# Kernel optimization log

Measured on AMD Instinct MI355X. Metric: run time of the kernel, lower is better.

Reference implementation:

```python
import jax, jax.numpy as jnp
import numpy as np

N, D, K, NCB = 65536, 256, 1024, 4


def setup_inputs() -> dict:
    key = jax.random.key(0)
    kz, kc = jax.random.split(key)
    z = jax.random.normal(kz, (N, D), dtype=jnp.float32)
    # nn.Embedding weights init: uniform(-1/k, 1/k)
    codebooks = jax.random.uniform(kc, (NCB, K, D), dtype=jnp.float32,
                                   minval=-1.0 / K, maxval=1.0 / K)
    return {"z": z, "codebooks": codebooks}


def _vq_step(r, W):
    """One VQ codebook pass. r: [N, D], W: [k, D].
    Squared L2 distance via matmul trick: ||r||^2 - 2 r.W^T + ||W||^2,
    same math as sum((r[:,None,:]-W)**2, -1) without the [N,k,D] blowup."""
    r2 = jnp.sum(r * r, axis=-1, keepdims=True)            # [N, 1]
    w2 = jnp.sum(W * W, axis=-1)                           # [k]
    dist = r2 - 2.0 * (r @ W.T) + w2                       # [N, k]
    ind = jnp.argmin(dist, axis=-1)                        # [N]
    z_q = W[ind]                                           # [N, D]
    sg = jax.lax.stop_gradient
    vq_loss = jnp.mean((z_q - sg(r)) ** 2)
    commitment_loss = jnp.mean((r - sg(z_q)) ** 2)
    z_q_st = r + sg(z_q - r)                               # straight-through
    return z_q_st, ind, vq_loss + commitment_loss


def reference(z, codebooks):
    residual = z
    quant_sum = jnp.zeros_like(z)
    inds = []
    total_loss = jnp.zeros((), dtype=z.dtype)
    for i in range(codebooks.shape[0]):  # small fixed loop over codebooks
        z_q, ind, loss = _vq_step(residual, codebooks[i])
        residual = residual - z_q
        quant_sum = quant_sum + z_q
        inds.append(ind)
        total_loss = total_loss + loss
    return quant_sum, jnp.stack(inds, axis=1), total_loss
```

## Files before the change

kernel.cpp:

```cpp
#include <hip/hip_runtime.h>


#define N_TOK 65536
#define DIM   256
#define KCB   1024
#define NCBK  4

#define TM  32
#define TK  512
#define DC  16
#define RST 260
#define WST 18

#define QS_F   ((size_t)N_TOK * DIM)
#define IDX_F  QS_F
#define IDXE_F (IDX_F + (size_t)N_TOK * NCBK)
#define LOSS_F IDXE_F

#define WS_PART_OFF 16384
#define WS_FLAG_OFF 32768

typedef unsigned short u16;
typedef unsigned int   u32;

__device__ __forceinline__ float bf2f(u32 h) { return __uint_as_float(h << 16); }

__device__ __forceinline__ float getv(const void* base, int f32in, size_t elt) {
    if (f32in) return ((const float*)base)[elt];
    return bf2f(((const u16*)base)[elt]);
}

__device__ __forceinline__ void load8(const void* base, int f32in, size_t elt,
                                      float* f) {
    if (f32in) {
        const float4* p = (const float4*)((const float*)base + elt);
        float4 a = p[0], b = p[1];
        f[0] = a.x; f[1] = a.y; f[2] = a.z; f[3] = a.w;
        f[4] = b.x; f[5] = b.y; f[6] = b.z; f[7] = b.w;
    } else {
        uint4 q = *(const uint4*)((const u16*)base + elt);
        f[0] = bf2f(q.x & 0xffffu); f[1] = bf2f(q.x >> 16);
        f[2] = bf2f(q.y & 0xffffu); f[3] = bf2f(q.y >> 16);
        f[4] = bf2f(q.z & 0xffffu); f[5] = bf2f(q.z >> 16);
        f[6] = bf2f(q.w & 0xffffu); f[7] = bf2f(q.w >> 16);
    }
}

__global__ void canary_kernel(float* out) {
    int gid = blockIdx.x * 256 + threadIdx.x;
    size_t pos = IDX_F + (size_t)gid;
    if (pos < IDXE_F) out[pos] = 512.0f;
    if (gid == 0) out[LOSS_F] = 512.0f;
}

__global__ void detect_kernel(const u16* z16, const u16* cb16, int* flags) {
    __shared__ int s0[256], s1[256];
    int tid = threadIdx.x;
    u32 a = z16[tid],  ea = (a >> 7) & 0xffu;
    u32 b = cb16[tid], eb = (b >> 7) & 0xffu;
    s0[tid] = ((ea >= 90u && ea <= 140u) || ((a & 0x7fffu) == 0u)) ? 1 : 0;
    s1[tid] = ((eb >= 90u && eb <= 140u) || ((b & 0x7fffu) == 0u)) ? 1 : 0;
    __syncthreads();
    for (int st = 128; st > 0; st >>= 1) {
        if (tid < st) { s0[tid] += s0[tid + st]; s1[tid] += s1[tid + st]; }
        __syncthreads();
    }
    if (tid == 0) { flags[0] = (s0[0] < 218) ? 1 : 0;
                    flags[1] = (s1[0] < 218) ? 1 : 0; }
}

__device__ __forceinline__ float np128_sq_g(const void* base, int f32in, size_t off) {
    float S[16];
    #pragma unroll
    for (int l = 0; l < 16; ++l) {
        float A[8];
        #pragma unroll
        for (int j = 0; j < 8; ++j) {
            float x = getv(base, f32in, off + 16 * j + l);
            A[j] = x * x;
        }
        S[l] = ((A[0] + A[1]) + (A[2] + A[3])) + ((A[4] + A[5]) + (A[6] + A[7]));
    }
    float B1[8], B2[4];
    #pragma unroll
    for (int l = 0; l < 8; ++l) B1[l] = S[l] + S[l + 8];
    #pragma unroll
    for (int l = 0; l < 4; ++l) B2[l] = B1[l] + B1[l + 4];
    return (B2[0] + B2[2]) + (B2[1] + B2[3]);
}

__device__ __forceinline__ float np128_sq_lds(const float* a) {
    float S[16];
    #pragma unroll
    for (int l = 0; l < 16; ++l) {
        float A[8];
        #pragma unroll
        for (int j = 0; j < 8; ++j) { float x = a[16 * j + l]; A[j] = x * x; }
        S[l] = ((A[0] + A[1]) + (A[2] + A[3])) + ((A[4] + A[5]) + (A[6] + A[7]));
    }
    float B1[8], B2[4];
    #pragma unroll
    for (int l = 0; l < 8; ++l) B1[l] = S[l] + S[l + 8];
    #pragma unroll
    for (int l = 0; l < 4; ++l) B2[l] = B1[l] + B1[l + 4];
    return (B2[0] + B2[2]) + (B2[1] + B2[3]);
}

__global__ void w2_kernel(const void* cbs, float* w2f, const int* flags) {
    int kf = blockIdx.x * 256 + threadIdx.x;
    const int fc = flags[1];
    size_t base = (size_t)kf * DIM;
    w2f[kf] = np128_sq_g(cbs, fc, base) + np128_sq_g(cbs, fc, base + 128);
}

__global__
__attribute__((amdgpu_flat_work_group_size(256, 256), amdgpu_waves_per_eu(2, 2)))
void rq_kernel(const void* z, const void* cbs, const float* w2f,
               float* out, double* partials, const int* flags) {
    __shared__ float  Rld[TM * RST];
    __shared__ float  Wld[TK * WST];
    __shared__ float  r2s[TM];
    __shared__ int    bestk[TM];
    __shared__ double dred[256];

    float* candv = Wld;
    int*   candi = (int*)(Wld + TM * 65);

    const int fz = flags[0], fc = flags[1];
    const int tid  = threadIdx.x;
    const int tx   = tid & 31;
    const int ty   = tid >> 5;
    const int rowg = ty & 3;
    const int cg   = ty >> 2;
    const int row0 = blockIdx.x * TM;

    const int stg_k0 = tid >> 1;
    const int stg_dp = (tid & 1) * 8;

    for (int it = 0; it < 4; ++it) {
        int flat = it * 256 + tid;
        int r = flat >> 5, c8 = flat & 31;
        float f[8];
        load8(z, fz, (size_t)(row0 + r) * DIM + c8 * 8, f);
        int base = r * RST + c8 * 8;
        #pragma unroll
        for (int e = 0; e < 8; ++e) Rld[base + e] = f[e];
    }
    double lsum = 0.0;

    for (int cb = 0; cb < NCBK; ++cb) {
        const size_t cbW = (size_t)cb * KCB * DIM;
        const float* w2c = w2f + cb * KCB;

        __syncthreads();
        if (tid < TM) {
            const float* a = &Rld[tid * RST];
            r2s[tid] = np128_sq_lds(a) + np128_sq_lds(a + 128);
        }
        __syncthreads();

        float bval[8]; int bidx[8];
        #pragma unroll
        for (int i = 0; i < 8; ++i) { bval[i] = __uint_as_float(0x7f7fffffu); bidx[i] = 0; }

        for (int kt = 0; kt < KCB / TK; ++kt) {
            float acc[8][8];
            #pragma unroll
            for (int i = 0; i < 8; ++i)
                #pragma unroll
                for (int j = 0; j < 8; ++j) acc[i][j] = 0.f;

            for (int dc = 0; dc < DIM / DC; ++dc) {
                __syncthreads();
                #pragma unroll
                for (int it = 0; it < 4; ++it) {
                    int k  = it * 128 + stg_k0;
                    float f[8];
                    load8(cbs, fc, cbW + (size_t)(kt * TK + k) * DIM + dc * DC + stg_dp, f);
                    int wb = k * WST + stg_dp;
                    *(float2*)&Wld[wb]     = make_float2(f[0], f[1]);
                    *(float2*)&Wld[wb + 2] = make_float2(f[2], f[3]);
                    *(float2*)&Wld[wb + 4] = make_float2(f[4], f[5]);
                    *(float2*)&Wld[wb + 6] = make_float2(f[6], f[7]);
                }
                __syncthreads();

                #pragma unroll
                for (int dd = 0; dd < DC / 4; ++dd) {
                    float av[8][4];
                    #pragma unroll
                    for (int i = 0; i < 8; ++i) {
                        const float4 va = *(const float4*)
                            &Rld[(rowg + 4 * i) * RST + dc * DC + dd * 4];
                        av[i][0] = va.x; av[i][1] = va.y;
                        av[i][2] = va.z; av[i][3] = va.w;
                    }
                    #pragma unroll
                    for (int j = 0; j < 8; ++j) {
                        const int c = tx + 32 * j + 256 * cg;
                        const float2* wp = (const float2*)&Wld[c * WST + dd * 4];
                        const float2 b01 = wp[0];
                        const float2 b23 = wp[1];
                        #pragma unroll
                        for (int i = 0; i < 8; ++i) {
                            float s = acc[i][j];
                            s = fmaf(av[i][0], b01.x, s);
                            s = fmaf(av[i][1], b01.y, s);
                            s = fmaf(av[i][2], b23.x, s);
                            s = fmaf(av[i][3], b23.y, s);
                            acc[i][j] = s;
                        }
                    }
                }
            }
            #pragma unroll
            for (int j = 0; j < 8; ++j) {
                const int k = kt * TK + tx + 32 * j + 256 * cg;
                const float w2k = w2c[k];
                #pragma unroll
                for (int i = 0; i < 8; ++i) {
                    float t2   = r2s[rowg + 4 * i] - 2.0f * acc[i][j];
                    float dist = t2 + w2k;
                    if (dist < bval[i] || (dist == bval[i] && k < bidx[i])) {
                        bval[i] = dist; bidx[i] = k;
                    }
                }
            }
        }
        __syncthreads();
        #pragma unroll
        for (int i = 0; i < 8; ++i) {
            int r = rowg + 4 * i;
            candv[r * 65 + tx + 32 * cg] = bval[i];
            candi[r * 65 + tx + 32 * cg] = bidx[i];
        }
        __syncthreads();
        if (tid < TM) {
            float best = candv[tid * 65];
            int   bi   = candi[tid * 65];
            for (int t = 1; t < 64; ++t) {
                float v = candv[tid * 65 + t];
                int  ix = candi[tid * 65 + t];
                if (v < best || (v == best && ix < bi)) { best = v; bi = ix; }
            }
            bestk[tid] = bi;
            size_t pos = IDX_F + (size_t)(row0 + tid) * NCBK + cb;
            if (pos < IDXE_F) out[pos] = (float)bi;
        }
        __syncthreads();
        #pragma unroll
        for (int it = 0; it < 4; ++it) {
            int flat = it * 256 + tid;
            int r = flat >> 5, c8 = flat & 31;
            int kb = bestk[r];
            float f[8];
            load8(cbs, fc, cbW + (size_t)kb * DIM + c8 * 8, f);
            int base = r * RST + c8 * 8;
            size_t pos = (size_t)(row0 + r) * DIM + c8 * 8;
            float qv[8];
            if (cb == 0) {
                #pragma unroll
                for (int e = 0; e < 8; ++e) qv[e] = 0.0f;
            } else {
                float4 o0 = *(const float4*)&out[pos];
                float4 o1 = *(const float4*)&out[pos + 4];
                qv[0] = o0.x; qv[1] = o0.y; qv[2] = o0.z; qv[3] = o0.w;
                qv[4] = o1.x; qv[5] = o1.y; qv[6] = o1.z; qv[7] = o1.w;
            }
            #pragma unroll
            for (int e = 0; e < 8; ++e) {
                float rv = Rld[base + e];
                float t  = f[e] - rv;
                float s  = rv + t;
                float rn = rv - s;
                Rld[base + e] = rn;
                qv[e] = qv[e] + s;
                lsum += (double)t * (double)t;
            }
            float4 w0 = make_float4(qv[0], qv[1], qv[2], qv[3]);
            float4 w1 = make_float4(qv[4], qv[5], qv[6], qv[7]);
            *(float4*)&out[pos]     = w0;
            *(float4*)&out[pos + 4] = w1;
        }
        __syncthreads();
    }

    dred[tid] = lsum;
    __syncthreads();
    for (int s = 128; s > 0; s >>= 1) {
        if (tid < s) dred[tid] += dred[tid + s];
        __syncthreads();
    }
    if (tid == 0) partials[blockIdx.x] = dred[0];
}

__global__ void loss_final(const double* partials, float* out) {
    __shared__ double sred[256];
    int tid = threadIdx.x;
    double s = 0.0;
    for (int q = 0; q < 8; ++q) s += partials[tid + 256 * q];
    sred[tid] = s;
    __syncthreads();
    for (int st = 128; st > 0; st >>= 1) {
        if (tid < st) sred[tid] += sred[tid + st];
        __syncthreads();
    }
    if (tid == 0)
        out[LOSS_F] = (float)(2.0 * sred[0] / 16777216.0);
}

extern "C" void kernel_launch(void* const* d_in, const int* in_sizes, int n_in,
                              void* d_out, int out_size, void* d_ws, size_t ws_size,
                              hipStream_t stream) {
    (void)n_in; (void)out_size; (void)ws_size;
    const void* z;
    const void* cbs;
    if (in_sizes[0] == 16777216) { z = d_in[0]; cbs = d_in[1]; }
    else                         { z = d_in[1]; cbs = d_in[0]; }

    float*  out      = (float*)d_out;
    float*  w2f      = (float*)d_ws;
    double* partials = (double*)((char*)d_ws + WS_PART_OFF);
    int*    flags    = (int*)((char*)d_ws + WS_FLAG_OFF);

    canary_kernel<<<1024, 256, 0, stream>>>(out);
    detect_kernel<<<1, 256, 0, stream>>>((const u16*)z, (const u16*)cbs, flags);
    w2_kernel<<<16, 256, 0, stream>>>(cbs, w2f, flags);
    rq_kernel<<<N_TOK / TM, 256, 0, stream>>>(z, cbs, w2f, out, partials, flags);
    loss_final<<<1, 256, 0, stream>>>(partials, out);
}
```

Before: 2.767 ms.

## Restructure distance GEMM to one row per lane with wave-uniform codebook loads

Replaces the LDS-staged codebook tiling with a scheme where each lane owns one token row (64 rows per block) and each wave streams its own quarter of the codebook straight from global memory. Codewords are wave-uniform, so the loads can be scalar or broadcast and are double-buffered in registers. This drops the per-chunk LDS staging and its barriers and doubles rows per block. The cost is much less register reuse (8 accumulators per thread), more global/L2 traffic for codebook reads, and an argmin merge across waves that no longer breaks ties toward the lowest index.

```diff
diff --git a/kernel.cpp b/kernel.cpp
--- a/kernel.cpp
+++ b/kernel.cpp
@@ -6,11 +6,8 @@
 #define KCB   1024
 #define NCBK  4
 
-#define TM  32
-#define TK  512
-#define DC  16
+#define TM  64
 #define RST 260
-#define WST 18
 
 #define QS_F   ((size_t)N_TOK * DIM)
 #define IDX_F  QS_F
@@ -113,31 +110,103 @@
     w2f[kf] = np128_sq_g(cbs, fc, base) + np128_sq_g(cbs, fc, base + 128);
 }
 
-__global__
-__attribute__((amdgpu_flat_work_group_size(256, 256), amdgpu_waves_per_eu(2, 2)))
+#define LOADB_F32(B, DDX) {                                                  \
+    const float* _p = cbf + (size_t)(DDX) * 4;                               \
+    B[0] = *(const float4*)(_p);                                             \
+    B[1] = *(const float4*)(_p + DIM);                                       \
+    B[2] = *(const float4*)(_p + 2 * DIM);                                   \
+    B[3] = *(const float4*)(_p + 3 * DIM);                                   \
+    B[4] = *(const float4*)(_p + 4 * DIM);                                   \
+    B[5] = *(const float4*)(_p + 5 * DIM);                                   \
+    B[6] = *(const float4*)(_p + 6 * DIM);                                   \
+    B[7] = *(const float4*)(_p + 7 * DIM); }
+
+__device__ __forceinline__ float4 bf4(const u16* p) {
+    uint2 r = *(const uint2*)p;
+    return make_float4(bf2f(r.x & 0xffffu), bf2f(r.x >> 16),
+                       bf2f(r.y & 0xffffu), bf2f(r.y >> 16));
+}
+
+#define LOADB_BF16(B, DDX) {                                                 \
+    const u16* _p = cbh + (size_t)(DDX) * 4;                                 \
+    B[0] = bf4(_p);           B[1] = bf4(_p + DIM);                          \
+    B[2] = bf4(_p + 2 * DIM); B[3] = bf4(_p + 3 * DIM);                      \
+    B[4] = bf4(_p + 4 * DIM); B[5] = bf4(_p + 5 * DIM);                      \
+    B[6] = bf4(_p + 6 * DIM); B[7] = bf4(_p + 7 * DIM); }
+
+#define TILE_LOOP(LOADB)                                                     \
+    for (int tile = 0; tile < 32; ++tile) {                                  \
+        const int code0 = wv * 256 + tile * 8;                               \
+        const float* cbf = (const float*)cbs + cbW + (size_t)code0 * DIM;    \
+        const u16*   cbh = (const u16*)cbs + cbW + (size_t)code0 * DIM;      \
+        (void)cbf; (void)cbh;                                                \
+        float acc[8];                                                        \
+        _Pragma("unroll")                                                    \
+        for (int j = 0; j < 8; ++j) acc[j] = 0.f;                            \
+        float4 bA[8], bB[8];                                                 \
+        LOADB(bA, 0)                                                         \
+        _Pragma("unroll 2")                                                  \
+        for (int dd2 = 0; dd2 < 32; ++dd2) {                                 \
+            const int d0 = dd2 * 2;                                          \
+            LOADB(bB, d0 + 1)                                                \
+            {                                                                \
+                const float4 av = *(const float4*)&Rld[lane * RST + d0 * 4]; \
+                _Pragma("unroll")                                            \
+                for (int j = 0; j < 8; ++j) {                                \
+                    float s = acc[j];                                        \
+                    s = fmaf(av.x, bA[j].x, s);                              \
+                    s = fmaf(av.y, bA[j].y, s);                              \
+                    s = fmaf(av.z, bA[j].z, s);                              \
+                    s = fmaf(av.w, bA[j].w, s);                              \
+                    acc[j] = s;                                              \
+                }                                                            \
+            }                                                                \
+            LOADB(bA, (d0 + 2) & 63)                                         \
+            {                                                                \
+                const float4 av =                                            \
+                    *(const float4*)&Rld[lane * RST + (d0 + 1) * 4];         \
+                _Pragma("unroll")                                            \
+                for (int j = 0; j < 8; ++j) {                                \
+                    float s = acc[j];                                        \
+                    s = fmaf(av.x, bB[j].x, s);                              \
+                    s = fmaf(av.y, bB[j].y, s);                              \
+                    s = fmaf(av.z, bB[j].z, s);                              \
+                    s = fmaf(av.w, bB[j].w, s);                              \
+                    acc[j] = s;                                              \
+                }                                                            \
+            }                                                                \
+        }                                                                    \
+        _Pragma("unroll")                                                    \
+        for (int j = 0; j < 8; ++j) {                                        \
+            const int c = code0 + j;                                         \
+            const float w2k = w2c[c];                                        \
+            const float t2 = r2v - 2.0f * acc[j];                            \
+            const float dist = t2 + w2k;                                     \
+            if (dist < bval || (dist == bval && c < bidx)) {                 \
+                bval = dist; bidx = c;                                       \
+            }                                                                \
+        }                                                                    \
+    }
+
+__global__ __launch_bounds__(256, 2)
 void rq_kernel(const void* z, const void* cbs, const float* w2f,
                float* out, double* partials, const int* flags) {
     __shared__ float  Rld[TM * RST];
-    __shared__ float  Wld[TK * WST];
-    __shared__ float  r2s[TM];
+    __shared__ float  candv[4 * 64];
+    __shared__ int    candi[4 * 64];
     __shared__ int    bestk[TM];
     __shared__ double dred[256];
 
-    float* candv = Wld;
-    int*   candi = (int*)(Wld + TM * 65);
-
     const int fz = flags[0], fc = flags[1];
     const int tid  = threadIdx.x;
-    const int tx   = tid & 31;
-    const int ty   = tid >> 5;
-    const int rowg = ty & 3;
-    const int cg   = ty >> 2;
+    const int lane = tid & 63;
+    const int wv   = __builtin_amdgcn_readfirstlane(tid >> 6);
     const int row0 = blockIdx.x * TM;
 
-    const int stg_k0 = tid >> 1;
-    const int stg_dp = (tid & 1) * 8;
-
-    for (int it = 0; it < 4; ++it) {
+    const int drow = tid >> 2;
+    const int dseg = (tid & 3) * 64;
+
+    for (int it = 0; it < 8; ++it) {
         int flat = it * 256 + tid;
         int r = flat >> 5, c8 = flat & 31;
         float f[8];
@@ -153,134 +222,67 @@
         const float* w2c = w2f + cb * KCB;
 
         __syncthreads();
-        if (tid < TM) {
-            const float* a = &Rld[tid * RST];
-            r2s[tid] = np128_sq_lds(a) + np128_sq_lds(a + 128);
-        }
-        __syncthreads();
-
-        float bval[8]; int bidx[8];
-        #pragma unroll
-        for (int i = 0; i < 8; ++i) { bval[i] = __uint_as_float(0x7f7fffffu); bidx[i] = 0; }
-
-        for (int kt = 0; kt < KCB / TK; ++kt) {
-            float acc[8][8];
+
+        const float* arow = &Rld[lane * RST];
+        const float r2v = np128_sq_lds(arow) + np128_sq_lds(arow + 128);
+
+        float bval = __uint_as_float(0x7f7fffffu);
+        int   bidx = 0;
+
+        if (fc) { TILE_LOOP(LOADB_F32) }
+        else    { TILE_LOOP(LOADB_BF16) }
+
+        candv[wv * 64 + lane] = bval;
+        candi[wv * 64 + lane] = bidx;
+        __syncthreads();
+        {
+            float best = candv[lane];
+            int   bi   = candi[lane];
             #pragma unroll
-            for (int i = 0; i < 8; ++i)
-                #pragma unroll
-                for (int j = 0; j < 8; ++j) acc[i][j] = 0.f;
-
-            for (int dc = 0; dc < DIM / DC; ++dc) {
-                __syncthreads();
-                #pragma unroll
-                for (int it = 0; it < 4; ++it) {
-                    int k  = it * 128 + stg_k0;
-                    float f[8];
-                    load8(cbs, fc, cbW + (size_t)(kt * TK + k) * DIM + dc * DC + stg_dp, f);
-                    int wb = k * WST + stg_dp;
-                    *(float2*)&Wld[wb]     = make_float2(f[0], f[1]);
-                    *(float2*)&Wld[wb + 2] = make_float2(f[2], f[3]);
-                    *(float2*)&Wld[wb + 4] = make_float2(f[4], f[5]);
-                    *(float2*)&Wld[wb + 6] = make_float2(f[6], f[7]);
-                }
-                __syncthreads();
-
-                #pragma unroll
-                for (int dd = 0; dd < DC / 4; ++dd) {
-                    float av[8][4];
-                    #pragma unroll
-                    for (int i = 0; i < 8; ++i) {
-                        const float4 va = *(const float4*)
-                            &Rld[(rowg + 4 * i) * RST + dc * DC + dd * 4];
-                        av[i][0] = va.x; av[i][1] = va.y;
-                        av[i][2] = va.z; av[i][3] = va.w;
-                    }
-                    #pragma unroll
-                    for (int j = 0; j < 8; ++j) {
-                        const int c = tx + 32 * j + 256 * cg;
-                        const float2* wp = (const float2*)&Wld[c * WST + dd * 4];
-                        const float2 b01 = wp[0];
-                        const float2 b23 = wp[1];
-                        #pragma unroll
-                        for (int i = 0; i < 8; ++i) {
-                            float s = acc[i][j];
-                            s = fmaf(av[i][0], b01.x, s);
-                            s = fmaf(av[i][1], b01.y, s);
-                            s = fmaf(av[i][2], b23.x, s);
-                            s = fmaf(av[i][3], b23.y, s);
-                            acc[i][j] = s;
-                        }
-                    }
-                }
+            for (int w = 1; w < 4; ++w) {
+                float v = candv[w * 64 + lane];
+                int  ci = candi[w * 64 + lane];
+                if (v < best) { best = v; bi = ci; }
             }
-            #pragma unroll
-            for (int j = 0; j < 8; ++j) {
-                const int k = kt * TK + tx + 32 * j + 256 * cg;
-                const float w2k = w2c[k];
-                #pragma unroll
-                for (int i = 0; i < 8; ++i) {
-                    float t2   = r2s[rowg + 4 * i] - 2.0f * acc[i][j];
-                    float dist = t2 + w2k;
-                    if (dist < bval[i] || (dist == bval[i] && k < bidx[i])) {
-                        bval[i] = dist; bidx[i] = k;
-                    }
-                }
+            if (tid < 64) {
+                bestk[lane] = bi;
+                size_t pos = IDX_F + (size_t)(row0 + lane) * NCBK + cb;
+                if (pos < IDXE_F) out[pos] = (float)bi;
             }
         }
         __syncthreads();
-        #pragma unroll
-        for (int i = 0; i < 8; ++i) {
-            int r = rowg + 4 * i;
-            candv[r * 65 + tx + 32 * cg] = bval[i];
-            candi[r * 65 + tx + 32 * cg] = bidx[i];
-        }
-        __syncthreads();
-        if (tid < TM) {
-            float best = candv[tid * 65];
-            int   bi   = candi[tid * 65];
-            for (int t = 1; t < 64; ++t) {
-                float v = candv[tid * 65 + t];
-                int  ix = candi[tid * 65 + t];
-                if (v < best || (v == best && ix < bi)) { best = v; bi = ix; }
+
+        {
+            const int kb = bestk[drow];
+            for (int it = 0; it < 8; ++it) {
+                const int off = dseg + it * 8;
+                float f[8];
+                load8(cbs, fc, cbW + (size_t)kb * DIM + off, f);
+                const int    base = drow * RST + off;
+                const size_t pos  = (size_t)(row0 + drow) * DIM + off;
+                float qv[8];
+                if (cb == 0) {
+                    #pragma unroll
+                    for (int e = 0; e < 8; ++e) qv[e] = 0.0f;
+                } else {
+                    float4 o0 = *(const float4*)&out[pos];
+                    float4 o1 = *(const float4*)&out[pos + 4];
+                    qv[0] = o0.x; qv[1] = o0.y; qv[2] = o0.z; qv[3] = o0.w;
+                    qv[4] = o1.x; qv[5] = o1.y; qv[6] = o1.z; qv[7] = o1.w;
+                }
+                #pragma unroll
+                for (int e = 0; e < 8; ++e) {
+                    float rv = Rld[base + e];
+                    float t  = f[e] - rv;
+                    float s  = rv + t;
+                    float rn = rv - s;
+                    Rld[base + e] = rn;
+                    qv[e] = qv[e] + s;
+                    lsum += (double)t * (double)t;
+                }
+                *(float4*)&out[pos]     = make_float4(qv[0], qv[1], qv[2], qv[3]);
+                *(float4*)&out[pos + 4] = make_float4(qv[4], qv[5], qv[6], qv[7]);
             }
-            bestk[tid] = bi;
-            size_t pos = IDX_F + (size_t)(row0 + tid) * NCBK + cb;
-            if (pos < IDXE_F) out[pos] = (float)bi;
-        }
-        __syncthreads();
-        #pragma unroll
-        for (int it = 0; it < 4; ++it) {
-            int flat = it * 256 + tid;
-            int r = flat >> 5, c8 = flat & 31;
-            int kb = bestk[r];
-            float f[8];
-            load8(cbs, fc, cbW + (size_t)kb * DIM + c8 * 8, f);
-            int base = r * RST + c8 * 8;
-            size_t pos = (size_t)(row0 + r) * DIM + c8 * 8;
-            float qv[8];
-            if (cb == 0) {
-                #pragma unroll
-                for (int e = 0; e < 8; ++e) qv[e] = 0.0f;
-            } else {
-                float4 o0 = *(const float4*)&out[pos];
-                float4 o1 = *(const float4*)&out[pos + 4];
-                qv[0] = o0.x; qv[1] = o0.y; qv[2] = o0.z; qv[3] = o0.w;
-                qv[4] = o1.x; qv[5] = o1.y; qv[6] = o1.z; qv[7] = o1.w;
-            }
-            #pragma unroll
-            for (int e = 0; e < 8; ++e) {
-                float rv = Rld[base + e];
-                float t  = f[e] - rv;
-                float s  = rv + t;
-                float rn = rv - s;
-                Rld[base + e] = rn;
-                qv[e] = qv[e] + s;
-                lsum += (double)t * (double)t;
-            }
-            float4 w0 = make_float4(qv[0], qv[1], qv[2], qv[3]);
-            float4 w1 = make_float4(qv[4], qv[5], qv[6], qv[7]);
-            *(float4*)&out[pos]     = w0;
-            *(float4*)&out[pos + 4] = w1;
         }
         __syncthreads();
     }
@@ -298,7 +300,7 @@
     __shared__ double sred[256];
     int tid = threadIdx.x;
     double s = 0.0;
-    for (int q = 0; q < 8; ++q) s += partials[tid + 256 * q];
+    for (int q = 0; q < 4; ++q) s += partials[tid + 256 * q];
     sred[tid] = s;
     __syncthreads();
     for (int st = 128; st > 0; st >>= 1) {
```

Result: slower. 7.486 ms (+170.6%).
